# Kernel optimization log

Measured on AMD Instinct MI355X. Metric: run time of the kernel, lower is better.

Reference implementation:

```python
import jax, jax.numpy as jnp
import numpy as np

LEADER_IDX = 0
SOCIAL_DIST = 1.5
COHESION = 0.8
B, N, T = 64, 64, 100


def setup_inputs() -> dict:
    key = jax.random.key(0)
    k1, k2, k3, k4, k5 = jax.random.split(key, 5)
    # trajectories: (x, y, vel, yaw, acc, yawvel)
    x = jax.random.normal(k1, (B, N, T, 6), dtype=jnp.float32) * 5.0
    # world_from_agent: per-agent SE(2) homogeneous transform (B, 3, 3)
    theta = jax.random.uniform(k2, (B,), minval=-np.pi, maxval=np.pi)
    c, s = jnp.cos(theta), jnp.sin(theta)
    trans = jax.random.normal(k3, (B, 2), dtype=jnp.float32) * 50.0
    wfa = (jnp.zeros((B, 3, 3), dtype=jnp.float32)
           .at[:, 0, 0].set(c).at[:, 0, 1].set(-s)
           .at[:, 1, 0].set(s).at[:, 1, 1].set(c)
           .at[:, :2, 2].set(trans).at[:, 2, 2].set(1.0))
    # externalized randomness of torch forward (randint over B-1 choices, rand<p)
    rand_idx = jax.random.randint(k4, (T * N, B), 0, B - 1, dtype=jnp.int32)
    drop_mask = jax.random.uniform(k5, (T * N, B)) < COHESION
    return {"x": x, "world_from_agent": wfa, "rand_idx": rand_idx, "drop_mask": drop_mask}


def reference(x, world_from_agent, rand_idx, drop_mask):
    pos = x[..., :2]                                   # (B, N, T, 2)
    R = world_from_agent[:, :2, :2]                    # (B, 2, 2)
    t = world_from_agent[:, :2, 2]                     # (B, 2)
    pos_g = jnp.einsum('bntj,bij->bnti', pos, R) + t[:, None, None, :]
    # leader positions are detached (no grad), but same value in fwd
    leader = (jnp.arange(B) == LEADER_IDX)[:, None, None, None]
    pos_g = jnp.where(leader, jax.lax.stop_gradient(pos_g), pos_g)
    # (B,N,T,2) -> (T,N,B,2) -> (T*N, B, 2)  (matches torch transpose(0,2).reshape)
    flat = jnp.transpose(pos_g, (2, 1, 0, 3)).reshape(T * N, B, 2)
    # pairwise euclidean distances via norm trick (avoids (TN,B,B,2) diff tensor)
    sq = jnp.sum(flat * flat, axis=-1)                 # (TN, B)
    d2 = sq[:, :, None] + sq[:, None, :] - 2.0 * jnp.einsum('tbd,tcd->tbc', flat, flat)
    dist = jnp.sqrt(jnp.maximum(d2, 1e-12))            # (TN, B, B)
    eye = jnp.eye(B, dtype=bool)
    dist = jnp.where(eye[None], jnp.inf, dist)         # mask self-distance
    min_nb = jnp.argmin(dist, axis=-1).astype(jnp.int32)      # (TN, B)
    # row b of neighbor_choices is [0..b-1, b+1..B-1]; gather at rand_idx ->
    # value = rand_idx + (rand_idx >= b)
    b_idx = jnp.arange(B, dtype=jnp.int32)[None, :]
    rand_nb = rand_idx + (rand_idx >= b_idx).astype(jnp.int32)
    nb = jnp.where(drop_mask, rand_nb, min_nb)         # (TN, B)
    nd = jnp.take_along_axis(dist, nb[..., None], axis=2)[..., 0]  # (TN, B)
    nd = jnp.transpose(nd.reshape(T, N, B), (2, 1, 0))  # (B, N, T)
    loss = jnp.mean((nd - SOCIAL_DIST) ** 2, axis=-1)   # (B, N)
    return loss
```

## Files before the change

### kernel.cpp

```cpp
#include <hip/hip_runtime.h>

#define BB 64
#define NN 64
#define TT 100
#define TQ 4
#define NTQ (TT / TQ)

__global__ __launch_bounds__(256) void social_slice_kernel(
    const float* __restrict__ x,
    const float* __restrict__ wfa,
    const int* __restrict__ rand_idx,
    const int* __restrict__ drop_mask,
    float* __restrict__ ws)
{
    const int n  = blockIdx.x & 63;
    const int tq = blockIdx.x >> 6;
    const int t0 = tq * TQ;

    __shared__ float2 S[TQ][BB + 1];
    __shared__ float  Rld[TQ][BB];

    {
        const int lb = threadIdx.x >> 2;
        const int k  = threadIdx.x & 3;
        const float* wp = wfa + lb * 9;
        const float r00 = wp[0], r01 = wp[1], tx = wp[2];
        const float r10 = wp[3], r11 = wp[4], ty = wp[5];
        const size_t xoff = (((size_t)lb * NN + n) * (size_t)TT + (size_t)(t0 + k)) * 6;
        const float2 p = *(const float2*)(x + xoff);
        const float gx = r00 * p.x + r01 * p.y + tx;
        const float gy = r10 * p.x + r11 * p.y + ty;
        S[k][lb] = make_float2(gx, gy);
    }
    __syncthreads();

    const int w = threadIdx.x >> 6;
    const int b = threadIdx.x & 63;
    const int t = t0 + w;
    const int s = t * NN + n;
    const size_t sb = (size_t)s * BB + b;
    const int r  = rand_idx[sb];
    const int dm = drop_mask[sb];

    const float2 g = S[w][b];
    const float gx = g.x, gy = g.y;

    const float INF = __int_as_float(0x7f800000);
    float m0 = INF, m1 = INF, m2 = INF, m3 = INF;
    #pragma unroll
    for (int i = 0; i < 16; ++i) {
        {
            const int c = i;
            const float2 q = S[w][c];
            const float dx = gx - q.x, dy = gy - q.y;
            float d2 = fmaf(dx, dx, dy * dy);
            d2 = (c == b) ? INF : d2;
            m0 = fminf(m0, d2);
        }
        {
            const int c = 16 + i;
            const float2 q = S[w][c];
            const float dx = gx - q.x, dy = gy - q.y;
            float d2 = fmaf(dx, dx, dy * dy);
            d2 = (c == b) ? INF : d2;
            m1 = fminf(m1, d2);
        }
        {
            const int c = 32 + i;
            const float2 q = S[w][c];
            const float dx = gx - q.x, dy = gy - q.y;
            float d2 = fmaf(dx, dx, dy * dy);
            d2 = (c == b) ? INF : d2;
            m2 = fminf(m2, d2);
        }
        {
            const int c = 48 + i;
            const float2 q = S[w][c];
            const float dx = gx - q.x, dy = gy - q.y;
            float d2 = fmaf(dx, dx, dy * dy);
            d2 = (c == b) ? INF : d2;
            m3 = fminf(m3, d2);
        }
    }
    const float best = fminf(fminf(m0, m1), fminf(m2, m3));

    const int rnb = r + (r >= b ? 1 : 0);
    const float sq  = fmaf(gx, gx, gy * gy);
    const float qx  = __shfl(gx, rnb);
    const float qy  = __shfl(gy, rnb);
    const float qsq = __shfl(sq, rnb);
    const float d2r = fmaf(-2.0f, fmaf(gx, qx, gy * qy), sq + qsq);

    const float d2sel = dm ? d2r : best;
    const float nd = sqrtf(fmaxf(d2sel, 1e-12f));
    const float diff = nd - 1.5f;
    Rld[w][b] = diff * diff;
    __syncthreads();

    if (w == 0) {
        const float sum4 = ((Rld[0][b] + Rld[1][b]) + Rld[2][b]) + Rld[3][b];
        ws[((size_t)tq * NN + n) * BB + b] = sum4;
    }
}

__global__ __launch_bounds__(256) void social_reduce_kernel(
    const float* __restrict__ ws,
    float* __restrict__ out)
{
    const int b = threadIdx.x & 63;
    const int n = blockIdx.x * 4 + (threadIdx.x >> 6);

    float acc = 0.f;
    #pragma unroll
    for (int tq = 0; tq < NTQ; ++tq)
        acc += ws[((size_t)tq * NN + n) * BB + b];
    out[b * NN + n] = acc * (1.0f / TT);
}

extern "C" void kernel_launch(void* const* d_in, const int* in_sizes, int n_in,
                              void* d_out, int out_size, void* d_ws, size_t ws_size,
                              hipStream_t stream) {
    const float* x = (const float*)d_in[0];
    const float* wfa = (const float*)d_in[1];
    const int* rand_idx = (const int*)d_in[2];
    const int* drop_mask = (const int*)d_in[3];
    float* out = (float*)d_out;
    float* ws = (float*)d_ws;

    social_slice_kernel<<<NTQ * NN, 256, 0, stream>>>(
        x, wfa, rand_idx, drop_mask, ws);
    social_reduce_kernel<<<NN / 4, 256, 0, stream>>>(ws, out);
}
```

Before: 70.49 us.

## Use unsigned-bit min trick for self-mask, vectorized LDS reads, wider reduce grid

Replaces the explicit self-index masking in the nearest-neighbour scan with an integer trick. Each float distance is reinterpreted as unsigned and decremented, so the zero self-distance wraps to the maximum value and loses every min. Shared-memory loads become float4, reading two candidates at once, and the row padding changes so those loads stay aligned. The reduce kernel now runs one block per agent with a four-way split over time chunks, trading a tiny kernel for more parallelism. Risk: any non-self pair at exactly zero distance would also be ignored, and the result then differs from the reference.

```diff
diff --git a/kernel.cpp b/kernel.cpp
--- a/kernel.cpp
+++ b/kernel.cpp
@@ -17,7 +17,7 @@
     const int tq = blockIdx.x >> 6;
     const int t0 = tq * TQ;
 
-    __shared__ float2 S[TQ][BB + 1];
+    __shared__ float2 S[TQ][BB + 2];
     __shared__ float  Rld[TQ][BB];
 
     {
@@ -45,44 +45,48 @@
     const float2 g = S[w][b];
     const float gx = g.x, gy = g.y;
 
-    const float INF = __int_as_float(0x7f800000);
-    float m0 = INF, m1 = INF, m2 = INF, m3 = INF;
+    unsigned m0 = 0xFFFFFFFFu, m1 = 0xFFFFFFFFu, m2 = 0xFFFFFFFFu, m3 = 0xFFFFFFFFu;
     #pragma unroll
-    for (int i = 0; i < 16; ++i) {
+    for (int i = 0; i < 8; ++i) {
         {
-            const int c = i;
-            const float2 q = S[w][c];
-            const float dx = gx - q.x, dy = gy - q.y;
-            float d2 = fmaf(dx, dx, dy * dy);
-            d2 = (c == b) ? INF : d2;
-            m0 = fminf(m0, d2);
+            const int c = 2 * i;
+            const float4 q = *(const float4*)&S[w][c];
+            const float dx0 = gx - q.x, dy0 = gy - q.y;
+            const float dx1 = gx - q.z, dy1 = gy - q.w;
+            const unsigned u0 = __float_as_uint(fmaf(dx0, dx0, dy0 * dy0)) - 1u;
+            const unsigned u1 = __float_as_uint(fmaf(dx1, dx1, dy1 * dy1)) - 1u;
+            m0 = min(m0, min(u0, u1));
         }
         {
-            const int c = 16 + i;
-            const float2 q = S[w][c];
-            const float dx = gx - q.x, dy = gy - q.y;
-            float d2 = fmaf(dx, dx, dy * dy);
-            d2 = (c == b) ? INF : d2;
-            m1 = fminf(m1, d2);
+            const int c = 16 + 2 * i;
+            const float4 q = *(const float4*)&S[w][c];
+            const float dx0 = gx - q.x, dy0 = gy - q.y;
+            const float dx1 = gx - q.z, dy1 = gy - q.w;
+            const unsigned u0 = __float_as_uint(fmaf(dx0, dx0, dy0 * dy0)) - 1u;
+            const unsigned u1 = __float_as_uint(fmaf(dx1, dx1, dy1 * dy1)) - 1u;
+            m1 = min(m1, min(u0, u1));
         }
         {
-            const int c = 32 + i;
-            const float2 q = S[w][c];
-            const float dx = gx - q.x, dy = gy - q.y;
-            float d2 = fmaf(dx, dx, dy * dy);
-            d2 = (c == b) ? INF : d2;
-            m2 = fminf(m2, d2);
+            const int c = 32 + 2 * i;
+            const float4 q = *(const float4*)&S[w][c];
+            const float dx0 = gx - q.x, dy0 = gy - q.y;
+            const float dx1 = gx - q.z, dy1 = gy - q.w;
+            const unsigned u0 = __float_as_uint(fmaf(dx0, dx0, dy0 * dy0)) - 1u;
+            const unsigned u1 = __float_as_uint(fmaf(dx1, dx1, dy1 * dy1)) - 1u;
+            m2 = min(m2, min(u0, u1));
         }
         {
-            const int c = 48 + i;
-            const float2 q = S[w][c];
-            const float dx = gx - q.x, dy = gy - q.y;
-            float d2 = fmaf(dx, dx, dy * dy);
-            d2 = (c == b) ? INF : d2;
-            m3 = fminf(m3, d2);
+            const int c = 48 + 2 * i;
+            const float4 q = *(const float4*)&S[w][c];
+            const float dx0 = gx - q.x, dy0 = gy - q.y;
+            const float dx1 = gx - q.z, dy1 = gy - q.w;
+            const unsigned u0 = __float_as_uint(fmaf(dx0, dx0, dy0 * dy0)) - 1u;
+            const unsigned u1 = __float_as_uint(fmaf(dx1, dx1, dy1 * dy1)) - 1u;
+            m3 = min(m3, min(u0, u1));
         }
     }
-    const float best = fminf(fminf(m0, m1), fminf(m2, m3));
+    const unsigned mu = min(min(m0, m1), min(m2, m3));
+    const float best = __uint_as_float(mu + 1u);
 
     const int rnb = r + (r >= b ? 1 : 0);
     const float sq  = fmaf(gx, gx, gy * gy);
@@ -107,14 +111,20 @@
     const float* __restrict__ ws,
     float* __restrict__ out)
 {
+    const int n = blockIdx.x;
+    const int w = threadIdx.x >> 6;
     const int b = threadIdx.x & 63;
-    const int n = blockIdx.x * 4 + (threadIdx.x >> 6);
 
     float acc = 0.f;
     #pragma unroll
-    for (int tq = 0; tq < NTQ; ++tq)
+    for (int tq = w; tq < NTQ; tq += 4)
         acc += ws[((size_t)tq * NN + n) * BB + b];
-    out[b * NN + n] = acc * (1.0f / TT);
+
+    __shared__ float R2[4][BB];
+    R2[w][b] = acc;
+    __syncthreads();
+    if (w == 0)
+        out[b * NN + n] = (((R2[0][b] + R2[1][b]) + R2[2][b]) + R2[3][b]) * (1.0f / TT);
 }
 
 extern "C" void kernel_launch(void* const* d_in, const int* in_sizes, int n_in,
@@ -129,5 +139,5 @@
 
     social_slice_kernel<<<NTQ * NN, 256, 0, stream>>>(
         x, wfa, rand_idx, drop_mask, ws);
-    social_reduce_kernel<<<NN / 4, 256, 0, stream>>>(ws, out);
+    social_reduce_kernel<<<NN, 256, 0, stream>>>(ws, out);
 }
```

Measured after the change: 71.25 us. About the same (+1.1%).
